# Kernel tuning notes

Measured on AMD Instinct MI355X. Metric: run time of the kernel, lower is better.

## Reference

```python
import jax, jax.numpy as jnp
import numpy as np

N = 100000        # num_nodes
E = 3200000       # num_edges
IN_C = 256        # in_channels (feature dim)
OUT_C = 128       # out_channels (embedding dim)
KAPPA = 0.95


def proj_norm_inf(W, kappa):
    """Row-wise projection of W onto the l-inf operator-norm ball of radius kappa:
    rows whose l1 norm exceeds kappa are projected (abs values onto the simplex
    of radius kappa via sort, signs restored). Matches projection_norm_inf."""
    a = jnp.abs(W)
    s = jnp.sign(W)
    rowsum = a.sum(axis=-1)                      # [rows]
    n = W.shape[-1]
    u = jnp.sort(a, axis=-1)[:, ::-1]            # descending
    css = jnp.cumsum(u, axis=-1) - kappa
    ind = jnp.arange(1, n + 1, dtype=W.dtype)
    cond = (u - css / ind) > 0                   # prefix-true pattern
    rho = jnp.sum(cond, axis=-1)                 # number of active coords (>=1 when rowsum>kappa)
    rho_safe = jnp.maximum(rho, 1)
    theta = jnp.take_along_axis(css, (rho_safe - 1)[:, None], axis=-1)[:, 0] / rho_safe.astype(W.dtype)
    w_proj = jnp.maximum(a - theta[:, None], 0.0) * s
    return jnp.where((rowsum > kappa)[:, None], w_proj, W)


def gcn_conv(x, W, src, dst, num_nodes):
    """PyG GCNConv (bias=False, normalize=True, add_self_loops=True):
    out = D^{-1/2} (A + I) D^{-1/2} (x @ W.T)"""
    loop = jnp.arange(num_nodes, dtype=src.dtype)
    src_f = jnp.concatenate([src, loop])
    dst_f = jnp.concatenate([dst, loop])
    ones = jnp.ones(src_f.shape[0], dtype=x.dtype)
    deg = jax.ops.segment_sum(ones, dst_f, num_segments=num_nodes)   # [N]
    dinv = jnp.where(deg > 0, jax.lax.rsqrt(jnp.maximum(deg, 1.0)), 0.0)
    norm = dinv[src_f] * dinv[dst_f]                                 # [E+N]
    h = x @ W.T                                                      # [N, OUT_C]
    msg = h[src_f] * norm[:, None]                                   # gather + scale
    return jax.ops.segment_sum(msg, dst_f, num_segments=num_nodes)   # scatter-add


def setup_inputs() -> dict:
    key = jax.random.key(0)
    k1, k2, k3, k4, k5 = jax.random.split(key, 5)
    features = jax.random.normal(k1, (N, IN_C), dtype=jnp.float32)
    edge_index = jax.random.randint(k2, (2, E), 0, N, dtype=jnp.int32)
    embeddings = 0.01 * jax.random.uniform(k3, (N, OUT_C), dtype=jnp.float32)
    # xavier_uniform-ish init for weights
    lim_c = float(np.sqrt(6.0 / (OUT_C + OUT_C)))
    lim_m = float(np.sqrt(6.0 / (IN_C + OUT_C)))
    W_conv = jax.random.uniform(k4, (OUT_C, OUT_C), dtype=jnp.float32, minval=-lim_c, maxval=lim_c)
    W_mlp = jax.random.uniform(k5, (OUT_C, IN_C), dtype=jnp.float32, minval=-lim_m, maxval=lim_m)
    return {"features": features, "edge_index": edge_index, "embeddings": embeddings,
            "W_conv": W_conv, "W_mlp": W_mlp}


def reference(features, edge_index, embeddings, W_conv, W_mlp):
    # SoftIGNN.forward: project conv weight, then one IGNN layer:
    # x = relu(GCNConv(embeddings, edge_index) + Linear(features))
    W_p = proj_norm_inf(W_conv, KAPPA)
    src, dst = edge_index[0], edge_index[1]
    agg = gcn_conv(embeddings, W_p, src, dst, N)     # [N, OUT_C]
    x = agg + features @ W_mlp.T                     # [N, OUT_C]
    return jax.nn.relu(x)
```

## Files before the change

kernel.cpp:

```cpp
#include <hip/hip_runtime.h>

#define KAPPA 0.95f

typedef __attribute__((ext_vector_type(8))) short short8;
typedef __attribute__((ext_vector_type(4))) float f32x4;
typedef __attribute__((ext_vector_type(2))) float f32x2;

static __device__ inline unsigned short f2bf(float f) {
    unsigned int u = __float_as_uint(f);
    unsigned int rounding = 0x7fffu + ((u >> 16) & 1u);
    u += rounding;
    return (unsigned short)(u >> 16);
}
static __device__ inline unsigned int pack2bf(float x, float y) {
    return (unsigned int)f2bf(x) | ((unsigned int)f2bf(y) << 16);
}

#define H_SCALE 4096.0f
#define BIN_CAP 10240

__global__ __launch_bounds__(128) void proj_kernel(const float* __restrict__ W,
                                                   unsigned short* __restrict__ Wp_bf) {
    const int r = blockIdx.x;
    const int tid = threadIdx.x;
    __shared__ float s[128];
    __shared__ float c[128];
    __shared__ int rho_s;

    const float w = W[r * 128 + tid];
    const float a = fabsf(w);
    s[tid] = a;
    if (tid == 0) rho_s = 0;
    __syncthreads();

    for (int k = 2; k <= 128; k <<= 1) {
        for (int j = k >> 1; j > 0; j >>= 1) {
            int ixj = tid ^ j;
            if (ixj > tid) {
                bool up = ((tid & k) == 0);
                float x = s[tid], y = s[ixj];
                if ((x > y) == up) { s[tid] = y; s[ixj] = x; }
            }
            __syncthreads();
        }
    }

    const float u = s[127 - tid];
    c[tid] = u;
    __syncthreads();
    for (int off = 1; off < 128; off <<= 1) {
        float add = (tid >= off) ? c[tid - off] : 0.f;
        __syncthreads();
        c[tid] += add;
        __syncthreads();
    }
    const float rowsum = c[127];
    const float css = c[tid] - KAPPA;
    if (u - css / (float)(tid + 1) > 0.f) atomicAdd(&rho_s, 1);
    __syncthreads();

    float out = w;
    if (rowsum > KAPPA) {
        int rho = max(rho_s, 1);
        float theta = (c[rho - 1] - KAPPA) / (float)rho;
        float m = fmaxf(a - theta, 0.f);
        out = (w > 0.f) ? m : ((w < 0.f) ? -m : 0.f);
    }
    Wp_bf[r * 128 + tid] = f2bf(out);
}

__global__ void convw_kernel(const float* __restrict__ Wm, unsigned short* __restrict__ Wbf,
                             int n) {
    int i = blockIdx.x * blockDim.x + threadIdx.x;
    if (i < n) Wbf[i] = f2bf(Wm[i]);
}

__global__ __launch_bounds__(256) void rhist_kernel(const int* __restrict__ dst,
                                                    int* __restrict__ l2c, int E, unsigned N,
                                                    int chunk) {
    __shared__ int hist[512];
    const int b = blockIdx.x;
    const int i0 = b * chunk;
    const int i1 = min(i0 + chunk, E);
    for (int t = threadIdx.x; t < 512; t += 256) hist[t] = 0;
    __syncthreads();
    for (int i = i0 + threadIdx.x; i < i1; i += 256) {
        unsigned g = ((unsigned)dst[i] * 512u) / N;
        atomicAdd(&hist[g], 1);
    }
    __syncthreads();
    for (int t = threadIdx.x; t < 512; t += 256) l2c[(t << 9) | b] = hist[t];
}

__global__ __launch_bounds__(256) void rsum_kernel(const int* __restrict__ l2c,
                                                   int* __restrict__ R) {
    __shared__ int tmp[256];
    const int g = blockIdx.x;
    int s = 0;
    for (int j = threadIdx.x; j < 512; j += 256) s += l2c[(g << 9) | j];
    tmp[threadIdx.x] = s;
    __syncthreads();
    for (int off = 128; off > 0; off >>= 1) {
        if (threadIdx.x < off) tmp[threadIdx.x] += tmp[threadIdx.x + off];
        __syncthreads();
    }
    if (threadIdx.x == 0) R[g] = tmp[0];
}

__global__ __launch_bounds__(512) void rowscan_kernel(const int* __restrict__ l2c,
                                                      const int* __restrict__ R,
                                                      int* __restrict__ l2base) {
    __shared__ int tmpR[512];
    __shared__ int tmp[512];
    const int g = blockIdx.x;
    const int tid = threadIdx.x;
    tmpR[tid] = R[tid];
    __syncthreads();
    for (int off = 1; off < 512; off <<= 1) {
        int add = (tid >= off) ? tmpR[tid - off] : 0;
        __syncthreads();
        tmpR[tid] += add;
        __syncthreads();
    }
    const int gbase = (g == 0) ? 0 : tmpR[g - 1];
    int v = l2c[(g << 9) | tid];
    tmp[tid] = v;
    __syncthreads();
    int val = v;
    for (int off = 1; off < 512; off <<= 1) {
        int add = (tid >= off) ? tmp[tid - off] : 0;
        __syncthreads();
        val += add;
        tmp[tid] = val;
        __syncthreads();
    }
    l2base[(g << 9) | tid] = gbase + val - v;
}

__global__ __launch_bounds__(256) void rpart_kernel(const int* __restrict__ src,
                                                    const int* __restrict__ dst,
                                                    const int* __restrict__ l2base,
                                                    unsigned* __restrict__ queue2, int E,
                                                    unsigned N, int chunk) {
    __shared__ int base[512];
    const int b = blockIdx.x;
    const int i0 = b * chunk;
    const int i1 = min(i0 + chunk, E);
    for (int t = threadIdx.x; t < 512; t += 256) base[t] = l2base[(t << 9) | b];
    __syncthreads();
    for (int i = i0 + threadIdx.x; i < i1; i += 256) {
        unsigned d = (unsigned)dst[i];
        unsigned s = (unsigned)src[i];
        unsigned g = (d * 512u) / N;
        unsigned v0g = (g * N + 511u) >> 9;
        int p = atomicAdd(&base[g], 1);
        queue2[p] = ((d - v0g) << 24) | s;
    }
}

__global__ __launch_bounds__(1024) void subfill_kernel(const unsigned* __restrict__ queue2,
                                                       const int* __restrict__ l2base,
                                                       int* __restrict__ csr_src,
                                                       int* __restrict__ counts,
                                                       int* __restrict__ cursor,
                                                       float* __restrict__ dinv,
                                                       unsigned* __restrict__ h8z, unsigned N,
                                                       int E) {
    __shared__ int cnt[256];
    __shared__ int ofs[256];
    __shared__ int stage[BIN_CAP];
    const int B = blockIdx.x;
    const int g = (B & 7) * 64 + (B >> 3);
    const int e0 = l2base[g << 9];
    const int e1 = (g == 511) ? E : l2base[(g + 1) << 9];
    const unsigned v0 = ((unsigned)g * N + 511u) >> 9;
    const unsigned v1 = min((((unsigned)g + 1u) * N + 511u) >> 9, N);
    const int nn = (int)(v1 - v0);
    const int tid = threadIdx.x;
    if (g == 511 && tid < 32) h8z[(size_t)N * 32 + tid] = 0u;
    if (tid < 256) cnt[tid] = 0;
    __syncthreads();
    for (int i = e0 + tid; i < e1; i += 1024) atomicAdd(&cnt[queue2[i] >> 24], 1);
    __syncthreads();
    int cp = 0;
    if (tid < 256) { cp = (cnt[tid] + 15) & ~15; ofs[tid] = cp; }
    __syncthreads();
    for (int off = 1; off < 256; off <<= 1) {
        int add = (tid < 256 && tid >= off) ? ofs[tid - off] : 0;
        __syncthreads();
        if (tid < 256) ofs[tid] += add;
        __syncthreads();
    }
    const int ptot = ofs[255];
    if (tid < nn) {
        int pexcl = ofs[tid] - cp;
        counts[v0 + tid] = cnt[tid];
        cursor[v0 + tid] = g * BIN_CAP + pexcl;
        dinv[v0 + tid] = rsqrtf((float)(cnt[tid] + 1));
    }
    __syncthreads();
    if (tid < 256) ofs[tid] -= cp;
    __syncthreads();
    const int sent = (int)(N * 8u);
    for (int t = tid; t < ptot; t += 1024) stage[t] = sent;
    __syncthreads();
    for (int i = e0 + tid; i < e1; i += 1024) {
        unsigned raw = queue2[i];
        int p = atomicAdd(&ofs[raw >> 24], 1);
        stage[p] = (int)((raw & 0xFFFFFFu) << 3);
    }
    __syncthreads();
    for (int t = tid; t < ptot; t += 1024) csr_src[g * BIN_CAP + t] = stage[t];
}

template <int KD, int MODE>
__global__ __launch_bounds__(512) void gemm_mfma(const float* __restrict__ X,
                                                 const unsigned short* __restrict__ Wbf,
                                                 const float* __restrict__ dinv,
                                                 const float* ADD,
                                                 unsigned int* __restrict__ out_u32,
                                                 float* out_f, int nrows) {
    __shared__ __align__(16) unsigned short ldsW[128 * KD];
    const int tid = threadIdx.x;
    const int w = tid >> 6;
    const int l = tid & 63;
    const int l16 = l & 15;
    const int kg = l >> 4;
    const unsigned swz = (unsigned)((l16 & 7) << 4);
    const int row0 = blockIdx.x * 128;
    const int row = row0 + w * 16 + l16;
    const int rload = min(row, nrows - 1);
    const float* xrow = X + (size_t)rload * KD + kg * 8;

    {
        const uint4* wsrc = reinterpret_cast<const uint4*>(Wbf);
        char* lb = reinterpret_cast<char*>(ldsW);
        constexpr int NCH = 128 * KD / 8;
#pragma unroll
        for (int i = 0; i < NCH / 512; ++i) {
            int idx = i * 512 + tid;
            int sidx = idx * 8;
            unsigned byte = (unsigned)(sidx * 2);
            byte ^= (unsigned)(((sidx / KD) & 7) << 4);
            *reinterpret_cast<uint4*>(lb + byte) = wsrc[idx];
        }
    }
    __syncthreads();

    f32x4 acc[8];
#pragma unroll
    for (int j = 0; j < 8; ++j) acc[j] = (f32x4)(0.f);

    const char* lbr = reinterpret_cast<const char*>(ldsW);
    constexpr int NT = KD / 32;
#pragma unroll
    for (int t = 0; t < NT; ++t) {
        const float4 v0 = *reinterpret_cast<const float4*>(xrow + t * 32);
        const float4 v1 = *reinterpret_cast<const float4*>(xrow + t * 32 + 4);
        union { uint4 u; short8 s; } cvt;
        cvt.u.x = pack2bf(v0.x, v0.y);
        cvt.u.y = pack2bf(v0.z, v0.w);
        cvt.u.z = pack2bf(v1.x, v1.y);
        cvt.u.w = pack2bf(v1.z, v1.w);
        const short8 a = cvt.s;
#pragma unroll
        for (int ct = 0; ct < 8; ++ct) {
            const int c = ct * 16 + l16;
            unsigned byte = (unsigned)((c * KD + t * 32 + kg * 8) * 2) ^ swz;
            short8 wv = *reinterpret_cast<const short8*>(lbr + byte);
            acc[ct] = __builtin_amdgcn_mfma_f32_16x16x32_bf16(wv, a, acc[ct], 0, 0, 0);
        }
    }

    if (row < nrows) {
        if (MODE == 0) {
            const float dv = dinv[row] * H_SCALE;
#pragma unroll
            for (int ct = 0; ct < 8; ++ct) {
                f32x4 d = acc[ct];
                unsigned lo = __builtin_amdgcn_cvt_pk_fp8_f32(d[0] * dv, d[1] * dv, 0u, false);
                unsigned hi = __builtin_amdgcn_cvt_pk_fp8_f32(d[2] * dv, d[3] * dv, lo, true);
                out_u32[(size_t)row * 32 + ct * 4 + kg] = hi;
            }
        } else {
#pragma unroll
            for (int ct = 0; ct < 8; ++ct) {
                f32x4 d = acc[ct];
                const float4 a =
                    *reinterpret_cast<const float4*>(&ADD[(size_t)row * 128 + ct * 16 + kg * 4]);
                float4 o;
                o.x = fmaxf(d[0] + a.x, 0.f);
                o.y = fmaxf(d[1] + a.y, 0.f);
                o.z = fmaxf(d[2] + a.z, 0.f);
                o.w = fmaxf(d[3] + a.w, 0.f);
                *reinterpret_cast<float4*>(&out_f[(size_t)row * 128 + ct * 16 + kg * 4]) = o;
            }
        }
    }
}

static __device__ inline void unp8v(f32x2* acc, unsigned wv, int off) {
    acc[off + 0] += __builtin_amdgcn_cvt_pk_f32_fp8(wv, false);
    acc[off + 1] += __builtin_amdgcn_cvt_pk_f32_fp8(wv, true);
}
static __device__ inline void unp16(f32x2* acc, uint4 val) {
    unp8v(acc, val.x, 0);
    unp8v(acc, val.y, 2);
    unp8v(acc, val.z, 4);
    unp8v(acc, val.w, 6);
}

__global__ __launch_bounds__(256) void agg_kernel(const uint4* __restrict__ h8,
                                                  const int* __restrict__ csr_src,
                                                  const int* __restrict__ cursor,
                                                  const int* __restrict__ counts,
                                                  const float* __restrict__ dinv,
                                                  float* __restrict__ agg, int n) {
    int v = blockIdx.x * 4 + (threadIdx.x >> 6);
    if (v >= n) return;
    const int lane = threadIdx.x & 63;
    const int eg = lane >> 3;
    const int c = lane & 7;
    const int cnt = counts[v];
    const int start = cursor[v];
    const int cnt_pad = (cnt + 15) & ~15;

    f32x2 acc[8];
#pragma unroll
    for (int j = 0; j < 8; ++j) acc[j] = (f32x2)(0.f);

    int s0 = csr_src[start + eg];
    int s1 = csr_src[start + 8 + eg];
    for (int base = 0; base < cnt_pad; base += 16) {
        int t0 = s0, t1 = s1;
        s0 = csr_src[start + base + 16 + eg];
        s1 = csr_src[start + base + 24 + eg];
        uint4 va = h8[t0 + c];
        uint4 vb = h8[t1 + c];
        unp16(acc, va);
        unp16(acc, vb);
    }
    {
        uint4 val = h8[(size_t)v * 8 + c];
        unp16(acc, val);
    }
#pragma unroll
    for (int j = 0; j < 8; ++j) {
#pragma unroll
        for (int k = 0; k < 2; ++k) {
            acc[j][k] += __shfl_xor(acc[j][k], 8);
            acc[j][k] += __shfl_xor(acc[j][k], 16);
            acc[j][k] += __shfl_xor(acc[j][k], 32);
        }
    }
    if (eg == 0) {
        const float dv = dinv[v] * (1.0f / H_SCALE);
#pragma unroll
        for (int k = 0; k < 4; ++k) {
            float4 o = {acc[2 * k][0] * dv, acc[2 * k][1] * dv, acc[2 * k + 1][0] * dv,
                        acc[2 * k + 1][1] * dv};
            *reinterpret_cast<float4*>(&agg[(size_t)v * 128 + c * 16 + k * 4]) = o;
        }
    }
}

extern "C" void kernel_launch(void* const* d_in, const int* in_sizes, int n_in,
                              void* d_out, int out_size, void* d_ws, size_t ws_size,
                              hipStream_t stream) {
    const float* features = (const float*)d_in[0];
    const int*   edge     = (const int*)d_in[1];
    const float* emb      = (const float*)d_in[2];
    const float* Wconv    = (const float*)d_in[3];
    const float* Wmlp     = (const float*)d_in[4];
    float* out = (float*)d_out;

    const int N = in_sizes[0] / 256;
    const int E = in_sizes[1] / 2;
    const int* src = edge;
    const int* dst = edge + E;
    const int chunk = (E + 511) / 512;

    char* ws = (char*)d_ws;
    size_t o = 0;
    auto take = [&](size_t b) {
        size_t cur = o;
        o += (b + 255) & ~(size_t)255;
        return cur;
    };
    unsigned short* Wp_bf   = (unsigned short*)(ws + take((size_t)128 * 128 * 2));
    unsigned short* Wm_bf   = (unsigned short*)(ws + take((size_t)128 * 256 * 2));
    int*            counts  = (int*)(ws + take((size_t)N * 4));
    int*            cursor  = (int*)(ws + take((size_t)N * 4));
    float*          dinv    = (float*)(ws + take((size_t)N * 4));
    int*            l2c     = (int*)(ws + take((size_t)512 * 512 * 4));
    int*            l2base  = (int*)(ws + take((size_t)512 * 512 * 4));
    int*            R       = (int*)(ws + take((size_t)512 * 4));
    int*            csr_src = (int*)(ws + take((size_t)512 * BIN_CAP * 4 + 256));
    size_t qbytes = (size_t)E * 4;
    size_t hbytes = (size_t)(N + 1) * 128;
    char*  qh     = ws + take(qbytes > hbytes ? qbytes : hbytes);
    unsigned*     queue2 = (unsigned*)qh;
    unsigned int* h8     = (unsigned int*)qh;
    (void)ws_size; (void)n_in; (void)out_size;

    hipLaunchKernelGGL(proj_kernel, dim3(128), dim3(128), 0, stream, Wconv, Wp_bf);
    hipLaunchKernelGGL(convw_kernel, dim3((128 * 256 + 255) / 256), dim3(256), 0, stream, Wmlp,
                       Wm_bf, 128 * 256);
    hipLaunchKernelGGL(rhist_kernel, dim3(512), dim3(256), 0, stream, dst, l2c, E, (unsigned)N,
                       chunk);
    hipLaunchKernelGGL(rsum_kernel, dim3(512), dim3(256), 0, stream, l2c, R);
    hipLaunchKernelGGL(rowscan_kernel, dim3(512), dim3(512), 0, stream, l2c, R, l2base);
    hipLaunchKernelGGL(rpart_kernel, dim3(512), dim3(256), 0, stream, src, dst, l2base, queue2, E,
                       (unsigned)N, chunk);
    hipLaunchKernelGGL(subfill_kernel, dim3(512), dim3(1024), 0, stream, queue2, l2base, csr_src,
                       counts, cursor, dinv, h8, (unsigned)N, E);
    hipLaunchKernelGGL((gemm_mfma<128, 0>), dim3((N + 127) / 128), dim3(512), 0, stream, emb,
                       Wp_bf, dinv, (const float*)nullptr, h8, (float*)nullptr, N);
    hipLaunchKernelGGL(agg_kernel, dim3((N + 3) / 4), dim3(256), 0, stream, (const uint4*)h8,
                       csr_src, cursor, counts, dinv, out, N);
    hipLaunchKernelGGL((gemm_mfma<256, 1>), dim3((N + 127) / 128), dim3(512), 0, stream, features,
                       Wm_bf, (const float*)nullptr, out, (unsigned int*)nullptr, out, N);
}
```

Baseline: 208.7 us.

## Stage radix partition in shared memory and write bucket runs contiguously

```diff
diff --git a/kernel.cpp b/kernel.cpp
--- a/kernel.cpp
+++ b/kernel.cpp
@@ -137,24 +137,51 @@
     l2base[(g << 9) | tid] = gbase + val - v;
 }
 
-__global__ __launch_bounds__(256) void rpart_kernel(const int* __restrict__ src,
-                                                    const int* __restrict__ dst,
-                                                    const int* __restrict__ l2base,
-                                                    unsigned* __restrict__ queue2, int E,
-                                                    unsigned N, int chunk) {
-    __shared__ int base[512];
+__global__ __launch_bounds__(1024) void rpart_kernel(const int* __restrict__ src,
+                                                     const int* __restrict__ dst,
+                                                     const int* __restrict__ l2c,
+                                                     const int* __restrict__ l2base,
+                                                     unsigned* __restrict__ queue2, int E,
+                                                     unsigned N, int chunk) {
+    __shared__ int cnt[512];
+    __shared__ int ofs[512];
+    __shared__ int cur[512];
+    __shared__ unsigned stage[8192];
     const int b = blockIdx.x;
     const int i0 = b * chunk;
     const int i1 = min(i0 + chunk, E);
-    for (int t = threadIdx.x; t < 512; t += 256) base[t] = l2base[(t << 9) | b];
-    __syncthreads();
-    for (int i = i0 + threadIdx.x; i < i1; i += 256) {
+    const int tid = threadIdx.x;
+    if (tid < 512) cnt[tid] = l2c[(tid << 9) | b];
+    __syncthreads();
+    if (tid < 512) ofs[tid] = cnt[tid];
+    __syncthreads();
+    for (int off = 1; off < 512; off <<= 1) {
+        int add = (tid < 512 && tid >= off) ? ofs[tid - off] : 0;
+        __syncthreads();
+        if (tid < 512) ofs[tid] += add;
+        __syncthreads();
+    }
+    if (tid < 512) {
+        int e = ofs[tid] - cnt[tid];
+        ofs[tid] = e;
+        cur[tid] = e;
+    }
+    __syncthreads();
+    for (int i = i0 + tid; i < i1; i += 1024) {
         unsigned d = (unsigned)dst[i];
         unsigned s = (unsigned)src[i];
         unsigned g = (d * 512u) / N;
         unsigned v0g = (g * N + 511u) >> 9;
-        int p = atomicAdd(&base[g], 1);
-        queue2[p] = ((d - v0g) << 24) | s;
+        int p = atomicAdd(&cur[g], 1);
+        stage[p] = ((d - v0g) << 24) | s;
+    }
+    __syncthreads();
+    const int wid = tid >> 6, lane = tid & 63;
+    for (int g = wid; g < 512; g += 16) {
+        const int base = l2base[(g << 9) | b];
+        const int o = ofs[g];
+        const int c = cnt[g];
+        for (int t = lane; t < c; t += 64) queue2[base + t] = stage[o + t];
     }
 }
 
@@ -410,8 +437,8 @@
                        chunk);
     hipLaunchKernelGGL(rsum_kernel, dim3(512), dim3(256), 0, stream, l2c, R);
     hipLaunchKernelGGL(rowscan_kernel, dim3(512), dim3(512), 0, stream, l2c, R, l2base);
-    hipLaunchKernelGGL(rpart_kernel, dim3(512), dim3(256), 0, stream, src, dst, l2base, queue2, E,
-                       (unsigned)N, chunk);
+    hipLaunchKernelGGL(rpart_kernel, dim3(512), dim3(1024), 0, stream, src, dst, l2c, l2base,
+                       queue2, E, (unsigned)N, chunk);
     hipLaunchKernelGGL(subfill_kernel, dim3(512), dim3(1024), 0, stream, queue2, l2base, csr_src,
                        counts, cursor, dinv, h8, (unsigned)N, E);
     hipLaunchKernelGGL((gemm_mfma<128, 0>), dim3((N + 127) / 128), dim3(512), 0, stream, emb,
```

Result: faster. 195.6 us (-6.3%).
